# Performance work log

Hardware: AMD Instinct MI355X
Metric: run time of the kernel (lower is better)

Reference implementation:

```python
import jax, jax.numpy as jnp
import numpy as np

N_HEAD, D_K, D_V, D_MODEL = 16, 64, 64, 1024
LN_EPS = 1e-5


def setup_inputs() -> dict:
    key = jax.random.key(0)
    ks = jax.random.split(key, 13)
    B, S = 2, 2048
    s = 1.0 / np.sqrt(D_MODEL)
    return {
        "q": jax.random.normal(ks[0], (B, S, D_MODEL), jnp.float32),
        "k": jax.random.normal(ks[1], (B, S, D_MODEL), jnp.float32),
        "v": jax.random.normal(ks[2], (B, S, D_MODEL), jnp.float32),
        "Wq": jax.random.normal(ks[3], (D_MODEL, N_HEAD * D_K), jnp.float32) * s,
        "bq": jnp.zeros((N_HEAD * D_K,), jnp.float32),
        "Wk": jax.random.normal(ks[4], (D_MODEL, N_HEAD * D_K), jnp.float32) * s,
        "bk": jnp.zeros((N_HEAD * D_K,), jnp.float32),
        "Wv": jax.random.normal(ks[5], (D_MODEL, N_HEAD * D_V), jnp.float32) * s,
        "bv": jnp.zeros((N_HEAD * D_V,), jnp.float32),
        "Wo": jax.random.normal(ks[6], (N_HEAD * D_V, D_MODEL), jnp.float32) * s,
        "bo": jnp.zeros((D_MODEL,), jnp.float32),
        "ln_gamma": jnp.ones((D_MODEL,), jnp.float32),
        "ln_beta": jnp.zeros((D_MODEL,), jnp.float32),
    }


def reference(q, k, v, Wq, bq, Wk, bk, Wv, bv, Wo, bo, ln_gamma, ln_beta):
    B, S, _ = q.shape
    temperature = jnp.asarray(np.power(D_K, 0.5), q.dtype)
    # QKV projections -> [B, S, H, d]
    q_ = (q @ Wq + bq).reshape(B, S, N_HEAD, D_K)
    k_ = (k @ Wk + bk).reshape(B, S, N_HEAD, D_K)
    v_ = (v @ Wv + bv).reshape(B, S, N_HEAD, D_V)
    # scaled dot-product attention per head
    scores = jnp.einsum("bqhd,bkhd->bhqk", q_, k_) / temperature
    attn = jax.nn.softmax(scores, axis=-1)
    ctx = jnp.einsum("bhqk,bkhd->bqhd", attn, v_).reshape(B, S, N_HEAD * D_V)
    # output projection + residual + LayerNorm
    out = ctx @ Wo + bo + q
    mu = jnp.mean(out, axis=-1, keepdims=True)
    var = jnp.var(out, axis=-1, keepdims=True)
    out = (out - mu) * jax.lax.rsqrt(var + LN_EPS) * ln_gamma + ln_beta
    return out
```

## Files before the change

kernel.cpp:

```cpp
#include <hip/hip_runtime.h>
#include <hip/hip_bf16.h>

typedef float f32x4 __attribute__((ext_vector_type(4)));
typedef float f32x16 __attribute__((ext_vector_type(16)));
typedef __bf16 bf16x8 __attribute__((ext_vector_type(8)));
typedef __bf16 bf16x4 __attribute__((ext_vector_type(4)));
typedef unsigned u32x2 __attribute__((ext_vector_type(2)));

#define DM 1024
#define SL 2048
#define NHEAD 16
#define LOG2E 1.44269504088896f
#define EXP2(x) __builtin_amdgcn_exp2f(x)

static __device__ __forceinline__ f32x4 mfma16(bf16x8 a, bf16x8 b, f32x4 c) {
    return __builtin_amdgcn_mfma_f32_16x16x32_bf16(a, b, c, 0, 0, 0);
}
static __device__ __forceinline__ f32x16 mfma32(bf16x8 a, bf16x8 b, f32x16 c) {
    return __builtin_amdgcn_mfma_f32_32x32x16_bf16(a, b, c, 0, 0, 0);
}

static __device__ __forceinline__ void gload16(const void* g, void* l) {
    __builtin_amdgcn_global_load_lds(
        (const __attribute__((address_space(1))) unsigned*)g,
        (__attribute__((address_space(3))) unsigned*)l, 16, 0, 0);
}

static __device__ __forceinline__ unsigned packbf(float lo, float hi) {
    unsigned short lu = __builtin_bit_cast(unsigned short, (__bf16)lo);
    unsigned short hu = __builtin_bit_cast(unsigned short, (__bf16)hi);
    return ((unsigned)hu << 16) | (unsigned)lu;
}

__global__ __launch_bounds__(256) void prep_kernel(
    const float* __restrict__ x0, const float* __restrict__ x1, const float* __restrict__ x2,
    __bf16* __restrict__ y0, __bf16* __restrict__ y1, __bf16* __restrict__ y2,
    const float* __restrict__ W0, const float* __restrict__ W1,
    const float* __restrict__ W2, const float* __restrict__ W3,
    __bf16* __restrict__ T0, __bf16* __restrict__ T1,
    __bf16* __restrict__ T2, __bf16* __restrict__ T3)
{
    const int bid = blockIdx.x;
    if (bid < 6144) {
        const int yy = bid >> 11, xx = bid & 2047;
        const float* x = (yy == 0) ? x0 : (yy == 1) ? x1 : x2;
        __bf16* y = (yy == 0) ? y0 : (yy == 1) ? y1 : y2;
        size_t i = ((size_t)xx * 256 + threadIdx.x) * 8;
        float4 a = *reinterpret_cast<const float4*>(&x[i]);
        float4 b = *reinterpret_cast<const float4*>(&x[i + 4]);
        bf16x8 o;
        o[0] = (__bf16)a.x; o[1] = (__bf16)a.y; o[2] = (__bf16)a.z; o[3] = (__bf16)a.w;
        o[4] = (__bf16)b.x; o[5] = (__bf16)b.y; o[6] = (__bf16)b.z; o[7] = (__bf16)b.w;
        *reinterpret_cast<bf16x8*>(&y[i]) = o;
    } else {
        __shared__ float tle[32][33];
        const int rem = bid - 6144;
        const int z = rem >> 10, r2 = rem & 1023;
        const int bx = r2 & 31, by = r2 >> 5;
        const float* W = (z == 0) ? W0 : (z == 1) ? W1 : (z == 2) ? W2 : W3;
        __bf16* Wt = (z == 0) ? T0 : (z == 1) ? T1 : (z == 2) ? T2 : T3;
        const int tx = threadIdx.x & 31, ty = threadIdx.x >> 5;
        const int n0 = bx * 32, k0 = by * 32;
#pragma unroll
        for (int i = 0; i < 4; ++i) {
            int r = ty + 8 * i;
            tle[r][tx] = W[(size_t)(k0 + r) * DM + (n0 + tx)];
        }
        __syncthreads();
#pragma unroll
        for (int i = 0; i < 4; ++i) {
            int r = ty + 8 * i;
            Wt[(size_t)(n0 + r) * DM + (k0 + tx)] = (__bf16)tle[tx][r];
        }
    }
}

static __device__ __forceinline__ void gemm64_body(
    const __bf16* __restrict__ A, const __bf16* __restrict__ Wt,
    const float* __restrict__ bias, const float* __restrict__ resid,
    __bf16* __restrict__ Yb, float* __restrict__ Yf,
    int mode, float oscale, int r0, int c0)
{
    __shared__ __attribute__((aligned(16))) __bf16 As[128 * 64];
    __shared__ __attribute__((aligned(16))) __bf16 Bs[64 * 64];
    const int t = threadIdx.x;
    const int w = t >> 6, lane = t & 63;
    const int l15 = lane & 15, lhi = lane >> 4;
    const int wr = w >> 1, wc = w & 1;
    const int lrow = lane >> 3;
    const int lcolswz = (((lane & 7) ^ lrow) << 3);
    const int jb = w * 4, jb2 = w * 2;
    const int swzr = (l15 & 7) << 3;

    const f32x4 fzero = {0.f, 0.f, 0.f, 0.f};
    f32x4 acc[4][2];
#pragma unroll
    for (int m = 0; m < 4; ++m)
#pragma unroll
        for (int n = 0; n < 2; ++n) acc[m][n] = fzero;

    const __bf16* gA = &A[(size_t)(r0 + jb * 8 + lrow) * DM + lcolswz];
    const __bf16* gB = &Wt[(size_t)(c0 + jb2 * 8 + lrow) * DM + lcolswz];

    for (int kt = 0; kt < DM; kt += 64) {
        __syncthreads();
#pragma unroll
        for (int i = 0; i < 4; ++i)
            gload16(gA + (size_t)i * 8 * DM + kt, &As[(jb + i) * 512]);
#pragma unroll
        for (int i = 0; i < 2; ++i)
            gload16(gB + (size_t)i * 8 * DM + kt, &Bs[(jb2 + i) * 512]);
        __syncthreads();
#pragma unroll
        for (int kk = 0; kk < 2; ++kk) {
            bf16x8 af[4], bfr[2];
#pragma unroll
            for (int m = 0; m < 4; ++m)
                af[m] = *reinterpret_cast<const bf16x8*>(
                    &As[(wr * 64 + m * 16 + l15) * 64 + ((kk * 32 + lhi * 8) ^ swzr)]);
#pragma unroll
            for (int n = 0; n < 2; ++n)
                bfr[n] = *reinterpret_cast<const bf16x8*>(
                    &Bs[(wc * 32 + n * 16 + l15) * 64 + ((kk * 32 + lhi * 8) ^ swzr)]);
#pragma unroll
            for (int m = 0; m < 4; ++m)
#pragma unroll
                for (int n = 0; n < 2; ++n)
                    acc[m][n] = mfma16(af[m], bfr[n], acc[m][n]);
        }
    }
    if (mode == 0) {
#pragma unroll
        for (int m = 0; m < 4; ++m)
#pragma unroll
            for (int n = 0; n < 2; ++n)
#pragma unroll
                for (int r = 0; r < 4; ++r) {
                    int grow = r0 + wr * 64 + m * 16 + lhi * 4 + r;
                    int gcol = c0 + wc * 32 + n * 16 + l15;
                    Yb[(size_t)grow * DM + gcol] =
                        (__bf16)((acc[m][n][r] + bias[gcol]) * oscale);
                }
    } else if (mode == 1) {
#pragma unroll
        for (int m = 0; m < 4; ++m)
#pragma unroll
            for (int n = 0; n < 2; ++n) {
                int token = r0 + wr * 64 + m * 16 + lhi * 4;
                int gcol = c0 + wc * 32 + n * 16 + l15;
                int bb = token >> 11, ss = token & (SL - 1);
                int hh = gcol >> 6, dd = gcol & 63;
                float bv = bias[gcol];
                bf16x4 pv;
#pragma unroll
                for (int r = 0; r < 4; ++r) pv[r] = (__bf16)(acc[m][n][r] + bv);
                *reinterpret_cast<bf16x4*>(
                    &Yb[(((size_t)(bb * NHEAD + hh)) * 64 + dd) * SL + ss]) = pv;
            }
    } else {
#pragma unroll
        for (int m = 0; m < 4; ++m)
#pragma unroll
            for (int n = 0; n < 2; ++n)
#pragma unroll
                for (int r = 0; r < 4; ++r) {
                    int grow = r0 + wr * 64 + m * 16 + lhi * 4 + r;
                    int gcol = c0 + wc * 32 + n * 16 + l15;
                    size_t idx = (size_t)grow * DM + gcol;
                    Yf[idx] = acc[m][n][r] + bias[gcol] + resid[idx];
                }
    }
}

__global__ __launch_bounds__(256) void qkv_kernel(
    const __bf16* __restrict__ xq, const __bf16* __restrict__ xk, const __bf16* __restrict__ xv,
    const __bf16* __restrict__ WtQ, const __bf16* __restrict__ WtK, const __bf16* __restrict__ WtV,
    const float* __restrict__ bq, const float* __restrict__ bk, const float* __restrict__ bv,
    __bf16* __restrict__ Qp, __bf16* __restrict__ Kp, __bf16* __restrict__ Vt)
{
    const int p = blockIdx.x;
    const int logical = (p & 7) * 192 + (p >> 3);
    const int x = logical & 15;
    const int s = logical >> 4;
    const int y = s & 31, z = s >> 5;
    const __bf16* X = (z == 0) ? xq : (z == 1) ? xk : xv;
    const __bf16* Wt = (z == 0) ? WtQ : (z == 1) ? WtK : WtV;
    const float* bias = (z == 0) ? bq : (z == 1) ? bk : bv;
    __bf16* Yb = (z == 0) ? Qp : (z == 1) ? Kp : Vt;
    int mode = (z == 2) ? 1 : 0;
    float oscale = (z == 0) ? (0.125f * LOG2E) : 1.0f;
    gemm64_body(X, Wt, bias, nullptr, Yb, nullptr, mode, oscale, y * 128, x * 64);
}

__global__ __launch_bounds__(256) void oproj_kernel(
    const __bf16* __restrict__ Cxb, const __bf16* __restrict__ WtO,
    const float* __restrict__ bo, const float* __restrict__ resid,
    float* __restrict__ pre)
{
    const int p = blockIdx.x;
    const int logical = (p & 7) * 64 + (p >> 3);
    const int x = logical & 15, y = logical >> 4;
    gemm64_body(Cxb, WtO, bo, resid, nullptr, pre, 2, 1.0f, y * 128, x * 64);
}

__global__ __launch_bounds__(512, 4) void attn_kernel(
    const __bf16* __restrict__ Qp, const __bf16* __restrict__ Kp,
    const __bf16* __restrict__ Vt, __bf16* __restrict__ Op, float2* __restrict__ ML)
{
    __shared__ __attribute__((aligned(16))) __bf16 Kl[2][4096];
    __shared__ __attribute__((aligned(16))) __bf16 Vl[2][4096];
    const int t = threadIdx.x;
    const int w = t >> 6, lane = t & 63;
    const int l31 = lane & 31, hi = lane >> 5;

    const int id = blockIdx.x;
    const int logical = (id & 7) * 96 + (id >> 3);
    const int part = logical >> 8;
    const int rem = logical & 255;
    const int bh = rem >> 3, qs = rem & 7;
    const int b = bh >> 4, h = bh & 15;
    const int t0 = (part * 32) / 3, t1 = ((part + 1) * 32) / 3;
    const size_t tokQ = (size_t)b * SL + qs * 256 + w * 32;
    const size_t kbase = (size_t)b * SL;
    const size_t vrow0 = (size_t)bh * 64;

    const int srow = t >> 3, scol = (t & 7) << 3;
    const __bf16* gK = &Kp[(kbase + srow) * DM + h * 64 + scol];
    const __bf16* gV = &Vt[(vrow0 + srow) * SL + scol];
    const int sidx = ((srow * 128 + scol * 2) ^ ((srow & 7) << 4)) >> 1;

    bf16x8 bq[4];
#pragma unroll
    for (int ks = 0; ks < 4; ++ks)
        bq[ks] = *reinterpret_cast<const bf16x8*>(
            &Qp[(tokQ + l31) * DM + h * 64 + ks * 16 + hi * 8]);

    f32x16 o0, o1;
#pragma unroll
    for (int r = 0; r < 16; ++r) { o0[r] = 0.f; o1[r] = 0.f; }
    float m_run = -1e30f, l_run = 0.f;

    const int swz = (l31 & 7) << 4;

    {
        bf16x8 kv = *reinterpret_cast<const bf16x8*>(gK + (size_t)t0 * 64 * DM);
        bf16x8 vv = *reinterpret_cast<const bf16x8*>(gV + t0 * 64);
        *reinterpret_cast<bf16x8*>(&Kl[0][sidx]) = kv;
        *reinterpret_cast<bf16x8*>(&Vl[0][sidx]) = vv;
    }

    for (int ti = t0; ti < t1; ++ti) {
        const int cb = (ti - t0) & 1;
        const bool pf = (ti + 1 < t1);
        bf16x8 kvn, vvn;
        if (pf) {
            kvn = *reinterpret_cast<const bf16x8*>(gK + (size_t)(ti + 1) * 64 * DM);
            vvn = *reinterpret_cast<const bf16x8*>(gV + (ti + 1) * 64);
        }
        __syncthreads();

        f32x16 c0, c1;
#pragma unroll
        for (int r = 0; r < 16; ++r) { c0[r] = 0.f; c1[r] = 0.f; }
        __builtin_amdgcn_s_setprio(1);
#pragma unroll
        for (int ks = 0; ks < 4; ++ks) {
            int off = ks * 32 + hi * 16;
            bf16x8 ak0 = *reinterpret_cast<const bf16x8*>(&Kl[cb][((l31 * 128 + off) ^ swz) >> 1]);
            bf16x8 ak1 = *reinterpret_cast<const bf16x8*>(&Kl[cb][(((32 + l31) * 128 + off) ^ swz) >> 1]);
            c0 = mfma32(ak0, bq[ks], c0);
            c1 = mfma32(ak1, bq[ks], c1);
        }
        __builtin_amdgcn_s_setprio(0);

        float mx[8];
#pragma unroll
        for (int r = 0; r < 8; ++r)
            mx[r] = fmaxf(fmaxf(c0[r], c0[r + 8]), fmaxf(c1[r], c1[r + 8]));
#pragma unroll
        for (int r = 0; r < 4; ++r) mx[r] = fmaxf(mx[r], mx[r + 4]);
        float tm = fmaxf(fmaxf(mx[0], mx[1]), fmaxf(mx[2], mx[3]));
        tm = fmaxf(tm, __shfl_xor(tm, 32));

        if (__any(tm > m_run + 11.5f)) {
            float nm = fmaxf(m_run, tm);
            float sc = EXP2(m_run - nm);
            m_run = nm;
            l_run *= sc;
#pragma unroll
            for (int r = 0; r < 16; ++r) {
                float sq = __shfl(sc, (r & 3) + 8 * (r >> 2) + 4 * hi);
                o0[r] *= sq; o1[r] *= sq;
            }
        }

        float s4a = 0.f, s4b = 0.f, s4c = 0.f, s4d = 0.f;
#pragma unroll
        for (int r = 0; r < 16; r += 4) {
            c0[r]     = EXP2(c0[r]     - m_run); s4a += c0[r];
            c0[r + 1] = EXP2(c0[r + 1] - m_run); s4b += c0[r + 1];
            c0[r + 2] = EXP2(c0[r + 2] - m_run); s4c += c0[r + 2];
            c0[r + 3] = EXP2(c0[r + 3] - m_run); s4d += c0[r + 3];
        }
#pragma unroll
        for (int r = 0; r < 16; r += 4) {
            c1[r]     = EXP2(c1[r]     - m_run); s4a += c1[r];
            c1[r + 1] = EXP2(c1[r + 1] - m_run); s4b += c1[r + 1];
            c1[r + 2] = EXP2(c1[r + 2] - m_run); s4c += c1[r + 2];
            c1[r + 3] = EXP2(c1[r + 3] - m_run); s4d += c1[r + 3];
        }
        float rs = (s4a + s4b) + (s4c + s4d);
        rs += __shfl_xor(rs, 32);
        l_run += rs;

        if (pf) {
            *reinterpret_cast<bf16x8*>(&Kl[cb ^ 1][sidx]) = kvn;
            *reinterpret_cast<bf16x8*>(&Vl[cb ^ 1][sidx]) = vvn;
        }

        unsigned wd0[8], wd1[8];
#pragma unroll
        for (int tt = 0; tt < 4; ++tt)
#pragma unroll
            for (int p = 0; p < 2; ++p) {
                wd0[tt * 2 + p] = packbf(c0[4 * tt + 2 * p], c0[4 * tt + 2 * p + 1]);
                wd1[tt * 2 + p] = packbf(c1[4 * tt + 2 * p], c1[4 * tt + 2 * p + 1]);
            }
        unsigned ua[4][4];
#pragma unroll
        for (int s = 0; s < 4; ++s) {
            int tA = (s & 1) * 2;
#pragma unroll
            for (int p = 0; p < 2; ++p) {
                unsigned va = (s < 2) ? wd0[tA * 2 + p] : wd1[tA * 2 + p];
                unsigned vb = (s < 2) ? wd0[(tA + 1) * 2 + p] : wd1[(tA + 1) * 2 + p];
                u32x2 rres = __builtin_amdgcn_permlane32_swap(va, vb, false, false);
                ua[s][p] = rres[0]; ua[s][2 + p] = rres[1];
            }
        }

        __builtin_amdgcn_s_setprio(1);
#pragma unroll
        for (int s = 0; s < 4; ++s) {
            bf16x8 as = *reinterpret_cast<const bf16x8*>(&ua[s][0]);
            bf16x8 vf0 = *reinterpret_cast<const bf16x8*>(
                &Vl[cb][((l31 * 128 + s * 32 + hi * 16) ^ swz) >> 1]);
            bf16x8 vf1 = *reinterpret_cast<const bf16x8*>(
                &Vl[cb][(((32 + l31) * 128 + s * 32 + hi * 16) ^ swz) >> 1]);
            o0 = mfma32(as, vf0, o0);
            o1 = mfma32(as, vf1, o1);
        }
        __builtin_amdgcn_s_setprio(0);
    }

    if (hi == 0)
        ML[((size_t)part * 4096 + tokQ + l31) * NHEAD + h] = float2{m_run, l_run};
    const size_t obase = (size_t)part * 4096 * DM;
#pragma unroll
    for (int r = 0; r < 16; ++r) {
        int qq = (r & 3) + 8 * (r >> 2) + 4 * hi;
        size_t rowi = obase + (tokQ + qq) * DM + h * 64;
        Op[rowi + l31]      = (__bf16)o0[r];
        Op[rowi + 32 + l31] = (__bf16)o1[r];
    }
}

__global__ __launch_bounds__(256) void combine_kernel(
    const __bf16* __restrict__ Op, const float2* __restrict__ ML,
    __bf16* __restrict__ Cxb)
{
    const size_t e = ((size_t)blockIdx.x * 256 + threadIdx.x) * 8;
    const int token = (int)(e >> 10);
    const int h = (int)((e >> 6) & 15);
    float2 ml0 = ML[(size_t)token * NHEAD + h];
    float2 ml1 = ML[((size_t)4096 + token) * NHEAD + h];
    float2 ml2 = ML[((size_t)8192 + token) * NHEAD + h];
    float M = fmaxf(fmaxf(ml0.x, ml1.x), ml2.x);
    float s0 = EXP2(ml0.x - M), s1 = EXP2(ml1.x - M), s2 = EXP2(ml2.x - M);
    float inv = 1.f / (ml0.y * s0 + ml1.y * s1 + ml2.y * s2);
    s0 *= inv; s1 *= inv; s2 *= inv;
    bf16x8 a0 = *reinterpret_cast<const bf16x8*>(&Op[e]);
    bf16x8 a1 = *reinterpret_cast<const bf16x8*>(&Op[(size_t)4096 * DM + e]);
    bf16x8 a2 = *reinterpret_cast<const bf16x8*>(&Op[(size_t)8192 * DM + e]);
    bf16x8 o;
#pragma unroll
    for (int j = 0; j < 8; ++j)
        o[j] = (__bf16)((float)a0[j] * s0 + (float)a1[j] * s1 + (float)a2[j] * s2);
    *reinterpret_cast<bf16x8*>(&Cxb[e]) = o;
}

__global__ __launch_bounds__(256) void ln_kernel(
    const float* __restrict__ X, const float* __restrict__ gamma,
    const float* __restrict__ beta, float* __restrict__ out)
{
    const int row = blockIdx.x, t = threadIdx.x;
    float4 v = *reinterpret_cast<const float4*>(&X[(size_t)row * DM + t * 4]);
    float s = v.x + v.y + v.z + v.w;
    float s2 = v.x * v.x + v.y * v.y + v.z * v.z + v.w * v.w;
#pragma unroll
    for (int off = 1; off < 64; off <<= 1) {
        s += __shfl_xor(s, off);
        s2 += __shfl_xor(s2, off);
    }
    __shared__ float rs[4], rs2[4];
    const int w = t >> 6;
    if ((t & 63) == 0) { rs[w] = s; rs2[w] = s2; }
    __syncthreads();
    s = rs[0] + rs[1] + rs[2] + rs[3];
    s2 = rs2[0] + rs2[1] + rs2[2] + rs2[3];
    float mean = s * (1.f / DM);
    float var = s2 * (1.f / DM) - mean * mean;
    float rstd = rsqrtf(var + 1e-5f);
    int c = t * 4;
    float4 o;
    o.x = (v.x - mean) * rstd * gamma[c + 0] + beta[c + 0];
    o.y = (v.y - mean) * rstd * gamma[c + 1] + beta[c + 1];
    o.z = (v.z - mean) * rstd * gamma[c + 2] + beta[c + 2];
    o.w = (v.w - mean) * rstd * gamma[c + 3] + beta[c + 3];
    *reinterpret_cast<float4*>(&out[(size_t)row * DM + c]) = o;
}

extern "C" void kernel_launch(void* const* d_in, const int* in_sizes, int n_in,
                              void* d_out, int out_size, void* d_ws, size_t ws_size,
                              hipStream_t stream) {
    (void)in_sizes; (void)n_in; (void)out_size; (void)ws_size;
    const float* q   = (const float*)d_in[0];
    const float* k   = (const float*)d_in[1];
    const float* v   = (const float*)d_in[2];
    const float* Wq  = (const float*)d_in[3];
    const float* bq  = (const float*)d_in[4];
    const float* Wk  = (const float*)d_in[5];
    const float* bk  = (const float*)d_in[6];
    const float* Wv  = (const float*)d_in[7];
    const float* bv  = (const float*)d_in[8];
    const float* Wo  = (const float*)d_in[9];
    const float* bo  = (const float*)d_in[10];
    const float* lng = (const float*)d_in[11];
    const float* lnb = (const float*)d_in[12];

    char* ws = (char*)d_ws;
    const size_t MB = (size_t)1 << 20;
    __bf16* WtQ = (__bf16*)(ws + 0 * MB);
    __bf16* WtK = (__bf16*)(ws + 2 * MB);
    __bf16* WtV = (__bf16*)(ws + 4 * MB);
    __bf16* WtO = (__bf16*)(ws + 6 * MB);
    __bf16* Xbq = (__bf16*)(ws + 8 * MB);
    __bf16* Xbk = (__bf16*)(ws + 16 * MB);
    __bf16* Xbv = (__bf16*)(ws + 24 * MB);
    __bf16* Qp  = (__bf16*)(ws + 32 * MB);
    __bf16* Kp  = (__bf16*)(ws + 40 * MB);
    __bf16* Vt  = (__bf16*)(ws + 48 * MB);
    __bf16* Cxb = (__bf16*)(ws + 56 * MB);
    float2* ML  = (float2*)(ws + 0 * MB);
    __bf16* Op  = (__bf16*)(ws + 8 * MB);
    float*  pre = (float*)(ws + 8 * MB);

    prep_kernel<<<dim3(10240), 256, 0, stream>>>(q, k, v, Xbq, Xbk, Xbv,
                                                 Wq, Wk, Wv, Wo, WtQ, WtK, WtV, WtO);

    qkv_kernel<<<dim3(1536), 256, 0, stream>>>(Xbq, Xbk, Xbv, WtQ, WtK, WtV,
                                               bq, bk, bv, Qp, Kp, Vt);
    attn_kernel<<<dim3(768), 512, 0, stream>>>(Qp, Kp, Vt, Op, ML);
    combine_kernel<<<dim3(2048), 256, 0, stream>>>(Op, ML, Cxb);
    oproj_kernel<<<dim3(512), 256, 0, stream>>>(Cxb, WtO, bo, q, pre);
    ln_kernel<<<4096, 256, 0, stream>>>(pre, lng, lnb, (float*)d_out);
}
```

Before: 141.0 us.

## Double-buffer GEMM LDS tiles and store pre-LayerNorm output in bf16

The shared GEMM body now uses two LDS buffers, so the async global-to-LDS load of the next K tile is issued while the current tile is consumed by MFMAs, with one barrier per iteration instead of two. Separately, the output projection writes its residual-added pre-LayerNorm result as bf16 instead of fp32, and the LayerNorm kernel reads bf16. This halves that intermediate traffic at the cost of precision before normalization. Doubling LDS per block to 48KB may reduce occupancy.

Result: slower. 146.6 us (+4.0%).

```diff
diff --git a/kernel.cpp b/kernel.cpp
--- a/kernel.cpp
+++ b/kernel.cpp
@@ -78,11 +78,11 @@
 static __device__ __forceinline__ void gemm64_body(
     const __bf16* __restrict__ A, const __bf16* __restrict__ Wt,
     const float* __restrict__ bias, const float* __restrict__ resid,
-    __bf16* __restrict__ Yb, float* __restrict__ Yf,
+    __bf16* __restrict__ Yb,
     int mode, float oscale, int r0, int c0)
 {
-    __shared__ __attribute__((aligned(16))) __bf16 As[128 * 64];
-    __shared__ __attribute__((aligned(16))) __bf16 Bs[64 * 64];
+    __shared__ __attribute__((aligned(16))) __bf16 As[2][128 * 64];
+    __shared__ __attribute__((aligned(16))) __bf16 Bs[2][64 * 64];
     const int t = threadIdx.x;
     const int w = t >> 6, lane = t & 63;
     const int l15 = lane & 15, lhi = lane >> 4;
@@ -102,32 +102,39 @@
     const __bf16* gA = &A[(size_t)(r0 + jb * 8 + lrow) * DM + lcolswz];
     const __bf16* gB = &Wt[(size_t)(c0 + jb2 * 8 + lrow) * DM + lcolswz];
 
-    for (int kt = 0; kt < DM; kt += 64) {
-        __syncthreads();
+    auto stage = [&](int buf, int kt) {
 #pragma unroll
         for (int i = 0; i < 4; ++i)
-            gload16(gA + (size_t)i * 8 * DM + kt, &As[(jb + i) * 512]);
+            gload16(gA + (size_t)i * 8 * DM + kt, &As[buf][(jb + i) * 512]);
 #pragma unroll
         for (int i = 0; i < 2; ++i)
-            gload16(gB + (size_t)i * 8 * DM + kt, &Bs[(jb2 + i) * 512]);
-        __syncthreads();
+            gload16(gB + (size_t)i * 8 * DM + kt, &Bs[buf][(jb2 + i) * 512]);
+    };
+
+    stage(0, 0);
+    __syncthreads();
+
+    for (int it = 0; it < DM / 64; ++it) {
+        const int cb = it & 1;
+        if (it + 1 < DM / 64) stage(cb ^ 1, (it + 1) * 64);
 #pragma unroll
         for (int kk = 0; kk < 2; ++kk) {
             bf16x8 af[4], bfr[2];
 #pragma unroll
             for (int m = 0; m < 4; ++m)
                 af[m] = *reinterpret_cast<const bf16x8*>(
-                    &As[(wr * 64 + m * 16 + l15) * 64 + ((kk * 32 + lhi * 8) ^ swzr)]);
+                    &As[cb][(wr * 64 + m * 16 + l15) * 64 + ((kk * 32 + lhi * 8) ^ swzr)]);
 #pragma unroll
             for (int n = 0; n < 2; ++n)
                 bfr[n] = *reinterpret_cast<const bf16x8*>(
-                    &Bs[(wc * 32 + n * 16 + l15) * 64 + ((kk * 32 + lhi * 8) ^ swzr)]);
+                    &Bs[cb][(wc * 32 + n * 16 + l15) * 64 + ((kk * 32 + lhi * 8) ^ swzr)]);
 #pragma unroll
             for (int m = 0; m < 4; ++m)
 #pragma unroll
                 for (int n = 0; n < 2; ++n)
                     acc[m][n] = mfma16(af[m], bfr[n], acc[m][n]);
         }
+        __syncthreads();
     }
     if (mode == 0) {
 #pragma unroll
@@ -167,7 +174,7 @@
                     int grow = r0 + wr * 64 + m * 16 + lhi * 4 + r;
                     int gcol = c0 + wc * 32 + n * 16 + l15;
                     size_t idx = (size_t)grow * DM + gcol;
-                    Yf[idx] = acc[m][n][r] + bias[gcol] + resid[idx];
+                    Yb[idx] = (__bf16)(acc[m][n][r] + bias[gcol] + resid[idx]);
                 }
     }
 }
@@ -189,18 +196,18 @@
     __bf16* Yb = (z == 0) ? Qp : (z == 1) ? Kp : Vt;
     int mode = (z == 2) ? 1 : 0;
     float oscale = (z == 0) ? (0.125f * LOG2E) : 1.0f;
-    gemm64_body(X, Wt, bias, nullptr, Yb, nullptr, mode, oscale, y * 128, x * 64);
+    gemm64_body(X, Wt, bias, nullptr, Yb, mode, oscale, y * 128, x * 64);
 }
 
 __global__ __launch_bounds__(256) void oproj_kernel(
     const __bf16* __restrict__ Cxb, const __bf16* __restrict__ WtO,
     const float* __restrict__ bo, const float* __restrict__ resid,
-    float* __restrict__ pre)
+    __bf16* __restrict__ pre)
 {
     const int p = blockIdx.x;
     const int logical = (p & 7) * 64 + (p >> 3);
     const int x = logical & 15, y = logical >> 4;
-    gemm64_body(Cxb, WtO, bo, resid, nullptr, pre, 2, 1.0f, y * 128, x * 64);
+    gemm64_body(Cxb, WtO, bo, resid, pre, 2, 1.0f, y * 128, x * 64);
 }
 
 __global__ __launch_bounds__(512, 4) void attn_kernel(
@@ -390,11 +397,12 @@
 }
 
 __global__ __launch_bounds__(256) void ln_kernel(
-    const float* __restrict__ X, const float* __restrict__ gamma,
+    const __bf16* __restrict__ X, const float* __restrict__ gamma,
     const float* __restrict__ beta, float* __restrict__ out)
 {
     const int row = blockIdx.x, t = threadIdx.x;
-    float4 v = *reinterpret_cast<const float4*>(&X[(size_t)row * DM + t * 4]);
+    bf16x4 v4 = *reinterpret_cast<const bf16x4*>(&X[(size_t)row * DM + t * 4]);
+    float4 v = {(float)v4[0], (float)v4[1], (float)v4[2], (float)v4[3]};
     float s = v.x + v.y + v.z + v.w;
     float s2 = v.x * v.x + v.y * v.y + v.z * v.z + v.w * v.w;
 #pragma unroll
@@ -453,7 +461,7 @@
     __bf16* Cxb = (__bf16*)(ws + 56 * MB);
     float2* ML  = (float2*)(ws + 0 * MB);
     __bf16* Op  = (__bf16*)(ws + 8 * MB);
-    float*  pre = (float*)(ws + 8 * MB);
+    __bf16* pre = (__bf16*)(ws + 8 * MB);
 
     prep_kernel<<<dim3(10240), 256, 0, stream>>>(q, k, v, Xbq, Xbk, Xbv,
                                                  Wq, Wk, Wv, Wo, WtQ, WtK, WtV, WtO);
```
